# Optimization experiments

Hardware: AMD Instinct MI355X
Metric: run time of the kernel (lower is better)

The kernel has to match this reference:

```python
import jax, jax.numpy as jnp
import numpy as np

H = 16  # n_head

def _rotate_half(x):
    d = x.shape[-1] // 2
    return jnp.concatenate([-x[..., d:], x[..., :d]], axis=-1)

def setup_inputs() -> dict:
    key = jax.random.key(0)
    ks = jax.random.split(key, 12)
    b, t, f, h = 8, 1024, 1024, H
    d = f // h
    inp = {
        "query": jax.random.normal(ks[0], (b, t, f), jnp.float32),
        "key": jax.random.normal(ks[1], (b, t, f), jnp.float32),
        "value": jax.random.normal(ks[2], (b, t, f), jnp.float32),
    }
    # realistic rotary cos/sin, shape (t,1,1,d_k)
    inv_freq = 1.0 / (10000.0 ** (np.arange(0, d, 2, dtype=np.float32) / d))
    pos = np.arange(t, dtype=np.float32)[:, None] * inv_freq[None, :]  # (t, d/2)
    emb = np.concatenate([pos, pos], axis=-1)  # (t, d)
    inp["cos"] = jnp.asarray(np.cos(emb)).reshape(t, 1, 1, d)
    inp["sin"] = jnp.asarray(np.sin(emb)).reshape(t, 1, 1, d)
    inp["mask"] = jax.random.randint(ks[3], (b, t, t), 0, 2) > 0
    s = 1.0 / np.sqrt(f)
    inp["Wq"] = jax.random.normal(ks[4], (f, f), jnp.float32) * s
    inp["bq"] = jax.random.normal(ks[5], (f,), jnp.float32) * 0.02
    inp["Wk"] = jax.random.normal(ks[6], (f, f), jnp.float32) * s
    inp["bk"] = jax.random.normal(ks[7], (f,), jnp.float32) * 0.02
    inp["Wv"] = jax.random.normal(ks[8], (f, f), jnp.float32) * s
    inp["bv"] = jax.random.normal(ks[9], (f,), jnp.float32) * 0.02
    inp["Wo"] = jax.random.normal(ks[10], (f, f), jnp.float32) * s
    inp["bo"] = jax.random.normal(ks[11], (f,), jnp.float32) * 0.02
    return inp

def reference(query, key, value, cos, sin, mask, Wq, bq, Wk, bk, Wv, bv, Wo, bo):
    b, t, f = query.shape
    h = H
    d = f // h
    # RoPE applied pre-projection, per-head layout (b,t,h,d)
    c = cos.reshape(1, t, 1, d)  # broadcast over batch and heads
    s = sin.reshape(1, t, 1, d)
    qr = query.reshape(b, t, h, d)
    kr = key.reshape(b, t, h, d)
    qr = qr * c + _rotate_half(qr) * s
    kr = kr * c + _rotate_half(kr) * s
    q_in = qr.reshape(b, t, f)
    k_in = kr.reshape(b, t, f)
    # QKV projections (nn.Linear: x @ W.T + b), then split heads -> (b,h,t,d)
    q = (jnp.einsum('btf,gf->btg', q_in, Wq) + bq).reshape(b, t, h, d).transpose(0, 2, 1, 3)
    k = (jnp.einsum('btf,gf->btg', k_in, Wk) + bk).reshape(b, t, h, d).transpose(0, 2, 1, 3)
    v = (jnp.einsum('btf,gf->btg', value, Wv) + bv).reshape(b, t, h, d).transpose(0, 2, 1, 3)
    scores = jnp.einsum('bhqd,bhkd->bhqk', q, k) / jnp.sqrt(jnp.asarray(d, q.dtype))
    m = mask[:, None, :, :]  # (b,1,t,t)
    scores = jnp.where(m, jnp.asarray(-10000.0, scores.dtype), scores)
    attn = jax.nn.softmax(scores, axis=-1)
    attn = jnp.where(m, jnp.asarray(0.0, attn.dtype), attn)
    out = jnp.einsum('bhqk,bhkd->bhqd', attn, v)  # (b,h,t,d)
    out = out.transpose(0, 2, 1, 3).reshape(b, t, f)
    return jnp.einsum('btf,gf->btg', out, Wo) + bo
```

## Files before the change

kernel.cpp:

```cpp
#include <hip/hip_runtime.h>
#include <stdint.h>

typedef short short8 __attribute__((ext_vector_type(8)));
typedef float f32x4 __attribute__((ext_vector_type(4)));
typedef unsigned short ushort4v __attribute__((ext_vector_type(4)));
typedef unsigned int uint4v __attribute__((ext_vector_type(4)));
typedef unsigned long long u64;

#if __has_builtin(__builtin_amdgcn_exp2f)
#define EXP2(x) __builtin_amdgcn_exp2f(x)
#else
#define EXP2(x) exp2f(x)
#endif

__device__ __forceinline__ unsigned short f2bf(float f) {
  union { float f; unsigned u; } v; v.f = f;
  unsigned r = v.u + 0x7fffu + ((v.u >> 16) & 1u);
  return (unsigned short)(r >> 16);
}

__device__ __forceinline__ unsigned cvt_pk_bf16(float lo, float hi) {
  unsigned r;
  asm("v_cvt_pk_bf16_f32 %0, %1, %2" : "=v"(r) : "v"(lo), "v"(hi));
  return r;
}

__device__ __forceinline__ void gld_lds16(const void* g, void* l) {
  __builtin_amdgcn_global_load_lds((const __attribute__((address_space(1))) void*)g,
                                   (__attribute__((address_space(3))) void*)l, 16, 0, 0);
}

__global__ void mask_pack(const int* __restrict__ mask, u64* __restrict__ bits) {
  const int tid = blockIdx.x * 256 + threadIdx.x;
  const int w = tid >> 6, j = tid & 63;
  const int gh = w & 1, ktb = (w >> 1) & 7, bq = w >> 4;
  const int nt = (j >> 2) & 7, r = j & 3, g = gh * 2 + (j >> 5);
  const int k = nt * 16 + g * 4 + r;
  const int v = mask[(size_t)bq * 1024 + ktb * 128 + k];
  const u64 b = __ballot(v != 0);
  if (j == 0) bits[w] = b;
}

__global__ void rope_cast_kernel(const float* __restrict__ q, const float* __restrict__ k,
                                 const float* __restrict__ v,
                                 const float* __restrict__ cs, const float* __restrict__ sn,
                                 unsigned short* __restrict__ qo, unsigned short* __restrict__ ko,
                                 unsigned short* __restrict__ vo) {
  const int idx = blockIdx.x * 256 + threadIdx.x;
  const int p   = idx & 7;
  const int bth = idx >> 3;
  const int t   = (bth >> 4) & 1023;
  const size_t base = (size_t)bth * 64;
  const int dd0 = p * 4;

  const float4 x0 = *(const float4*)(q + base + dd0);
  const float4 x1 = *(const float4*)(q + base + dd0 + 32);
  const float4 y0 = *(const float4*)(k + base + dd0);
  const float4 y1 = *(const float4*)(k + base + dd0 + 32);
  const float4 c0 = *(const float4*)(cs + t * 64 + dd0);
  const float4 c1 = *(const float4*)(cs + t * 64 + dd0 + 32);
  const float4 s0 = *(const float4*)(sn + t * 64 + dd0);
  const float4 s1 = *(const float4*)(sn + t * 64 + dd0 + 32);

  ushort4v qlo, qhi, klo, khi;
  qlo[0]=f2bf(x0.x*c0.x - x1.x*s0.x); qlo[1]=f2bf(x0.y*c0.y - x1.y*s0.y);
  qlo[2]=f2bf(x0.z*c0.z - x1.z*s0.z); qlo[3]=f2bf(x0.w*c0.w - x1.w*s0.w);
  qhi[0]=f2bf(x1.x*c1.x + x0.x*s1.x); qhi[1]=f2bf(x1.y*c1.y + x0.y*s1.y);
  qhi[2]=f2bf(x1.z*c1.z + x0.z*s1.z); qhi[3]=f2bf(x1.w*c1.w + x0.w*s1.w);
  klo[0]=f2bf(y0.x*c0.x - y1.x*s0.x); klo[1]=f2bf(y0.y*c0.y - y1.y*s0.y);
  klo[2]=f2bf(y0.z*c0.z - y1.z*s0.z); klo[3]=f2bf(y0.w*c0.w - y1.w*s0.w);
  khi[0]=f2bf(y1.x*c1.x + y0.x*s1.x); khi[1]=f2bf(y1.y*c1.y + y0.y*s1.y);
  khi[2]=f2bf(y1.z*c1.z + y0.z*s1.z); khi[3]=f2bf(y1.w*c1.w + y0.w*s1.w);

  *(ushort4v*)(qo + base + dd0)      = qlo;
  *(ushort4v*)(qo + base + dd0 + 32) = qhi;
  *(ushort4v*)(ko + base + dd0)      = klo;
  *(ushort4v*)(ko + base + dd0 + 32) = khi;

  const size_t vb = (size_t)idx * 8;
  const float4 va = *(const float4*)(v + vb);
  const float4 vbv = *(const float4*)(v + vb + 4);
  ushort4v oa, ob;
  oa[0]=f2bf(va.x); oa[1]=f2bf(va.y); oa[2]=f2bf(va.z); oa[3]=f2bf(va.w);
  ob[0]=f2bf(vbv.x); ob[1]=f2bf(vbv.y); ob[2]=f2bf(vbv.z); ob[3]=f2bf(vbv.w);
  *(ushort4v*)(vo + vb)     = oa;
  *(ushort4v*)(vo + vb + 4) = ob;
}

__global__ void cast4_kernel(const float* __restrict__ s0, const float* __restrict__ s1,
                             const float* __restrict__ s2, const float* __restrict__ s3,
                             unsigned short* __restrict__ d0, unsigned short* __restrict__ d1,
                             unsigned short* __restrict__ d2, unsigned short* __restrict__ d3) {
  const int m = blockIdx.y;
  const float* src = (m == 0) ? s0 : (m == 1) ? s1 : (m == 2) ? s2 : s3;
  unsigned short* dst = (m == 0) ? d0 : (m == 1) ? d1 : (m == 2) ? d2 : d3;
  const int i = blockIdx.x * 256 + threadIdx.x;
  const float4 v = *(const float4*)(src + (size_t)i * 4);
  ushort4v o;
  o[0]=f2bf(v.x); o[1]=f2bf(v.y); o[2]=f2bf(v.z); o[3]=f2bf(v.w);
  *(ushort4v*)(dst + (size_t)i * 4) = o;
}

__global__ __launch_bounds__(256, 4) void gemm_qkv(
    const unsigned short* __restrict__ Aq, const unsigned short* __restrict__ Ak,
    const unsigned short* __restrict__ Av,
    const unsigned short* __restrict__ Bq, const unsigned short* __restrict__ Bk,
    const unsigned short* __restrict__ Bv,
    const float* __restrict__ bq, const float* __restrict__ bk, const float* __restrict__ bv,
    unsigned short* __restrict__ Cq, unsigned short* __restrict__ Ck,
    unsigned short* __restrict__ Cv) {
  constexpr int K = 1024;
  const int z = blockIdx.z;
  const unsigned short* A  = (z == 0) ? Aq : (z == 1) ? Ak : Av;
  const unsigned short* Bw = (z == 0) ? Bq : (z == 1) ? Bk : Bv;
  const float* bias        = (z == 0) ? bq : (z == 1) ? bk : bv;
  unsigned short* Co       = (z == 0) ? Cq : (z == 1) ? Ck : Cv;
  const float scale = (z == 0) ? 0.18033688f : 1.0f;

  const int tid = threadIdx.x;
  const int wave = tid >> 6, lane = tid & 63;
  const int m0 = blockIdx.x * 128, n0 = blockIdx.y * 128;
  __shared__ unsigned short Asm[128 * 64];
  __shared__ unsigned short Bsm[128 * 64];
  f32x4 acc[4][4] = {};
  const int wr = (wave >> 1) * 64, wc = (wave & 1) * 64;
  const int ld_row = lane >> 3;
  const int ld_col = ((lane & 7) ^ ld_row) * 8;
  const int fr = lane & 15, g = lane >> 4;
  const int fr7 = fr & 7;

  for (int k0 = 0; k0 < K; k0 += 64) {
#pragma unroll
    for (int j = 0; j < 4; ++j) {
      const int c = j * 4 + wave;
      gld_lds16(A  + (size_t)(m0 + 8 * c + ld_row) * K + k0 + ld_col, &Asm[c * 512]);
      gld_lds16(Bw + (size_t)(n0 + 8 * c + ld_row) * K + k0 + ld_col, &Bsm[c * 512]);
    }
    __syncthreads();
#pragma unroll
    for (int ks = 0; ks < 2; ++ks) {
      const int ch = ((ks * 4 + g) ^ fr7) * 8;
      short8 af[4], bf[4];
#pragma unroll
      for (int i = 0; i < 4; ++i)
        af[i] = *(const short8*)&Asm[(wr + i * 16 + fr) * 64 + ch];
#pragma unroll
      for (int i = 0; i < 4; ++i)
        bf[i] = *(const short8*)&Bsm[(wc + i * 16 + fr) * 64 + ch];
#pragma unroll
      for (int i = 0; i < 4; ++i)
#pragma unroll
        for (int j = 0; j < 4; ++j)
          acc[i][j] = __builtin_amdgcn_mfma_f32_16x16x32_bf16(af[i], bf[j], acc[i][j], 0, 0, 0);
    }
    __syncthreads();
  }

#pragma unroll
  for (int i = 0; i < 4; ++i) {
    const int row_base = m0 + wr + i * 16 + g * 4;
#pragma unroll
    for (int j = 0; j < 4; ++j) {
      const int col = n0 + wc + j * 16 + fr;
      const float bval = bias[col];
      const int h_i = col >> 6, dd = col & 63;
      if (z < 2) {
#pragma unroll
        for (int r = 0; r < 4; ++r) {
          const int row = row_base + r;
          const int b_i = row >> 10, t_i = row & 1023;
          Co[((size_t)(b_i * 16 + h_i) * 1024 + t_i) * 64 + dd] = f2bf((acc[i][j][r] + bval) * scale);
        }
      } else {
#pragma unroll
        for (int r = 0; r < 4; ++r) {
          const int row = row_base + r;
          const int b_i = row >> 10, t_i = row & 1023;
          const int kk = t_i & 127;
          const int kp = ((kk >> 4) & 3) * 32 + ((kk >> 2) & 3) * 8 + ((kk >> 6) & 1) * 4 + (kk & 3);
          Co[((size_t)(b_i * 16 + h_i) * 64 + dd) * 1024 + (t_i & ~127) + kp] =
              f2bf((acc[i][j][r] + bval));
        }
      }
    }
  }
}

__global__ __launch_bounds__(256, 2) void gemm_o(
    const unsigned short* __restrict__ A, const unsigned short* __restrict__ Bw,
    const float* __restrict__ bias, float* __restrict__ C) {
  constexpr int K = 1024, N = 1024;
  const int tid = threadIdx.x;
  const int wave = tid >> 6, lane = tid & 63;
  const int m0 = blockIdx.x * 128, n0 = blockIdx.y * 128;
  __shared__ unsigned short Asm[128 * 64];
  __shared__ unsigned short Bsm[128 * 64];
  f32x4 acc[4][4] = {};
  const int wr = (wave >> 1) * 64, wc = (wave & 1) * 64;
  const int ld_row = lane >> 3;
  const int ld_col = ((lane & 7) ^ ld_row) * 8;
  const int fr = lane & 15, g = lane >> 4;
  const int fr7 = fr & 7;

  for (int k0 = 0; k0 < K; k0 += 64) {
#pragma unroll
    for (int j = 0; j < 4; ++j) {
      const int c = j * 4 + wave;
      gld_lds16(A  + (size_t)(m0 + 8 * c + ld_row) * K + k0 + ld_col, &Asm[c * 512]);
      gld_lds16(Bw + (size_t)(n0 + 8 * c + ld_row) * K + k0 + ld_col, &Bsm[c * 512]);
    }
    __syncthreads();
#pragma unroll
    for (int ks = 0; ks < 2; ++ks) {
      const int ch = ((ks * 4 + g) ^ fr7) * 8;
      short8 af[4], bf[4];
#pragma unroll
      for (int i = 0; i < 4; ++i)
        af[i] = *(const short8*)&Asm[(wr + i * 16 + fr) * 64 + ch];
#pragma unroll
      for (int i = 0; i < 4; ++i)
        bf[i] = *(const short8*)&Bsm[(wc + i * 16 + fr) * 64 + ch];
#pragma unroll
      for (int i = 0; i < 4; ++i)
#pragma unroll
        for (int j = 0; j < 4; ++j)
          acc[i][j] = __builtin_amdgcn_mfma_f32_16x16x32_bf16(af[i], bf[j], acc[i][j], 0, 0, 0);
    }
    __syncthreads();
  }

#pragma unroll
  for (int i = 0; i < 4; ++i) {
    const int row_base = m0 + wr + i * 16 + g * 4;
#pragma unroll
    for (int j = 0; j < 4; ++j) {
      const int col = n0 + wc + j * 16 + fr;
      const float bval = bias[col];
#pragma unroll
      for (int r = 0; r < 4; ++r)
        C[(size_t)(row_base + r) * N + col] = acc[i][j][r] + bval;
    }
  }
}

__global__ __launch_bounds__(256, 2) void flash_attn(
    const unsigned short* __restrict__ Qp, const unsigned short* __restrict__ Kp,
    const unsigned short* __restrict__ Vp, const u64* __restrict__ mbits,
    unsigned short* __restrict__ O) {
  const int bh = blockIdx.x & 127, b_i = bh >> 4, h_i = bh & 15;
  const int q0 = (blockIdx.x >> 7) * 128;
  const int tid = threadIdx.x, wave = tid >> 6, lane = tid & 63;
  const unsigned short* Qb = Qp + (size_t)bh * 65536;
  const unsigned short* Kb = Kp + (size_t)bh * 65536;
  const unsigned short* Vb = Vp + (size_t)bh * 65536;
  const u64* mb = mbits + (size_t)b_i * 16384;

  __shared__ unsigned short smem[16384];
  unsigned short* Vsm = smem;
  unsigned short* Ksm = smem + 8192;

  const int fr = lane & 15, g = lane >> 4, fr7 = fr & 7;
  const int qw = q0 + wave * 32;

  short8 qf[2][2];
#pragma unroll
  for (int mt = 0; mt < 2; ++mt)
#pragma unroll
    for (int ks = 0; ks < 2; ++ks)
      qf[mt][ks] = *(const short8*)&Qb[(size_t)(qw + mt * 16 + fr) * 64 + ks * 32 + g * 8];

  f32x4 o_acc[2][4] = {};
  f32x4 o_l[2] = {};
  const short8 ones = {0x3F80, 0x3F80, 0x3F80, 0x3F80, 0x3F80, 0x3F80, 0x3F80, 0x3F80};

  const int kld_row = lane >> 3;
  const int kld_col = ((lane & 7) ^ kld_row) * 8;
  const int vld_row = lane >> 4;
  const int vld_r7w = 4 * (wave & 1) + vld_row;
  const int vld_col = ((lane & 15) ^ vld_r7w) * 8;

  for (int kt = 0; kt < 1024; kt += 128) {
#pragma unroll
    for (int j = 0; j < 4; ++j) {
      const int c = j * 4 + wave;
      gld_lds16(Kb + (size_t)(kt + 8 * c + kld_row) * 64 + kld_col, &Ksm[c * 512]);
      gld_lds16(Vb + (size_t)(4 * c + vld_row) * 1024 + kt + vld_col, &Vsm[c * 512]);
    }
    __syncthreads();

    f32x4 s_acc[2][8] = {};
#pragma unroll
    for (int ks = 0; ks < 2; ++ks) {
      const int ch = ((ks * 4 + g) ^ fr7) * 8;
      short8 kf[8];
#pragma unroll
      for (int nt = 0; nt < 8; ++nt)
        kf[nt] = *(const short8*)&Ksm[(nt * 16 + fr) * 64 + ch];
      __builtin_amdgcn_s_setprio(1);
#pragma unroll
      for (int mt = 0; mt < 2; ++mt)
#pragma unroll
        for (int nt = 0; nt < 8; ++nt)
          s_acc[mt][nt] = __builtin_amdgcn_mfma_f32_16x16x32_bf16(kf[nt], qf[mt][ks], s_acc[mt][nt], 0, 0, 0);
      __builtin_amdgcn_s_setprio(0);
    }

    short8 pf[2][4];
#pragma unroll
    for (int mt = 0; mt < 2; ++mt) {
      const u64 w = mb[(size_t)(qw + mt * 16 + fr) * 16 + (kt >> 7) * 2 + (g >> 1)];
      const unsigned bits = (unsigned)(w >> ((g & 1) * 32));
#pragma unroll
      for (int ks2 = 0; ks2 < 4; ++ks2) {
        float e[8];
#pragma unroll
        for (int r = 0; r < 4; ++r) {
          float a = EXP2(s_acc[mt][ks2][r]);
          a = (bits & (1u << (ks2 * 4 + r))) ? 0.0f : a;
          float b2 = EXP2(s_acc[mt][ks2 + 4][r]);
          b2 = (bits & (1u << (16 + ks2 * 4 + r))) ? 0.0f : b2;
          e[r] = a; e[4 + r] = b2;
        }
        uint4v pk;
        pk[0] = cvt_pk_bf16(e[0], e[1]);
        pk[1] = cvt_pk_bf16(e[2], e[3]);
        pk[2] = cvt_pk_bf16(e[4], e[5]);
        pk[3] = cvt_pk_bf16(e[6], e[7]);
        union { uint4v u; short8 s; } cv; cv.u = pk;
        pf[mt][ks2] = cv.s;
      }
    }

#pragma unroll
    for (int ks2 = 0; ks2 < 4; ++ks2) {
      const int cc = (ks2 * 4 + g) ^ fr7;
      short8 vf[4];
#pragma unroll
      for (int dt = 0; dt < 4; ++dt)
        vf[dt] = *(const short8*)&Vsm[(dt * 16 + fr) * 128 + cc * 8];
      __builtin_amdgcn_s_setprio(1);
#pragma unroll
      for (int mt = 0; mt < 2; ++mt) {
#pragma unroll
        for (int dt = 0; dt < 4; ++dt)
          o_acc[mt][dt] = __builtin_amdgcn_mfma_f32_16x16x32_bf16(pf[mt][ks2], vf[dt], o_acc[mt][dt], 0, 0, 0);
        o_l[mt] = __builtin_amdgcn_mfma_f32_16x16x32_bf16(pf[mt][ks2], ones, o_l[mt], 0, 0, 0);
      }
      __builtin_amdgcn_s_setprio(0);
    }
    __syncthreads();
  }

#pragma unroll
  for (int mt = 0; mt < 2; ++mt) {
#pragma unroll
    for (int r = 0; r < 4; ++r) {
      const float inv_l = 1.0f / o_l[mt][r];
      const int qrow = qw + mt * 16 + g * 4 + r;
#pragma unroll
      for (int dt = 0; dt < 4; ++dt) {
        const int dcol = dt * 16 + fr;
        O[((size_t)(b_i * 1024 + qrow)) * 1024 + h_i * 64 + dcol] = f2bf(o_acc[mt][dt][r] * inv_l);
      }
    }
  }
}

extern "C" void kernel_launch(void* const* d_in, const int* in_sizes, int n_in,
                              void* d_out, int out_size, void* d_ws, size_t ws_size,
                              hipStream_t stream) {
  const float* query = (const float*)d_in[0];
  const float* key   = (const float*)d_in[1];
  const float* value = (const float*)d_in[2];
  const float* cosb  = (const float*)d_in[3];
  const float* sinb  = (const float*)d_in[4];
  const int*   mask  = (const int*)d_in[5];
  const float* Wq = (const float*)d_in[6];
  const float* bq = (const float*)d_in[7];
  const float* Wk = (const float*)d_in[8];
  const float* bk = (const float*)d_in[9];
  const float* Wv = (const float*)d_in[10];
  const float* bv = (const float*)d_in[11];
  const float* Wo = (const float*)d_in[12];
  const float* bo = (const float*)d_in[13];
  (void)in_sizes; (void)n_in; (void)out_size; (void)ws_size;

  char* ws = (char*)d_ws;
  const size_t MB = 1024 * 1024;
  unsigned short* q_in = (unsigned short*)(ws);
  unsigned short* k_in = (unsigned short*)(ws + 16 * MB);
  unsigned short* v_bf = (unsigned short*)(ws + 32 * MB);
  unsigned short* Qp   = (unsigned short*)(ws + 48 * MB);
  unsigned short* Kp   = (unsigned short*)(ws + 64 * MB);
  unsigned short* Vp   = (unsigned short*)(ws + 80 * MB);
  unsigned short* Wqb  = (unsigned short*)(ws + 96 * MB);
  unsigned short* Wkb  = (unsigned short*)(ws + 98 * MB);
  unsigned short* Wvb  = (unsigned short*)(ws + 100 * MB);
  unsigned short* Wob  = (unsigned short*)(ws + 102 * MB);
  u64*            mbits= (u64*)(ws + 104 * MB);
  unsigned short* attn = q_in;

  mask_pack<<<32768, 256, 0, stream>>>(mask, mbits);
  rope_cast_kernel<<<4096, 256, 0, stream>>>(query, key, value, cosb, sinb, q_in, k_in, v_bf);
  cast4_kernel<<<dim3(1024, 4), 256, 0, stream>>>(Wq, Wk, Wv, Wo, Wqb, Wkb, Wvb, Wob);

  dim3 blk(256);
  gemm_qkv<<<dim3(64, 8, 3), blk, 0, stream>>>(q_in, k_in, v_bf, Wqb, Wkb, Wvb,
                                               bq, bk, bv, Qp, Kp, Vp);
  flash_attn<<<1024, blk, 0, stream>>>(Qp, Kp, Vp, mbits, attn);
  gemm_o<<<dim3(64, 8), blk, 0, stream>>>(attn, Wob, bo, (float*)d_out);
}
```

Measured before the change: 343.3 us.

## Fuse prep kernels, double-buffer K/V tiles in attention, raise gemm_o occupancy

Merges the mask packing, RoPE/cast and weight-cast kernels into a single launch to cut launch overhead and tail gaps. The flash attention kernel now double-buffers its K/V shared-memory tiles, prefetching the next tile with async global-to-LDS loads and using explicit waitcnt and barriers. It also loads the mask words earlier in each iteration. gemm_o's launch bounds rise to 4 waves per SIMD, which may force register spills, and doubling LDS in attention may lower its occupancy.

```diff
diff --git a/kernel.cpp b/kernel.cpp
--- a/kernel.cpp
+++ b/kernel.cpp
@@ -30,75 +30,77 @@
                                    (__attribute__((address_space(3))) void*)l, 16, 0, 0);
 }
 
-__global__ void mask_pack(const int* __restrict__ mask, u64* __restrict__ bits) {
-  const int tid = blockIdx.x * 256 + threadIdx.x;
-  const int w = tid >> 6, j = tid & 63;
-  const int gh = w & 1, ktb = (w >> 1) & 7, bq = w >> 4;
-  const int nt = (j >> 2) & 7, r = j & 3, g = gh * 2 + (j >> 5);
-  const int k = nt * 16 + g * 4 + r;
-  const int v = mask[(size_t)bq * 1024 + ktb * 128 + k];
-  const u64 b = __ballot(v != 0);
-  if (j == 0) bits[w] = b;
-}
-
-__global__ void rope_cast_kernel(const float* __restrict__ q, const float* __restrict__ k,
-                                 const float* __restrict__ v,
-                                 const float* __restrict__ cs, const float* __restrict__ sn,
-                                 unsigned short* __restrict__ qo, unsigned short* __restrict__ ko,
-                                 unsigned short* __restrict__ vo) {
-  const int idx = blockIdx.x * 256 + threadIdx.x;
-  const int p   = idx & 7;
-  const int bth = idx >> 3;
-  const int t   = (bth >> 4) & 1023;
-  const size_t base = (size_t)bth * 64;
-  const int dd0 = p * 4;
-
-  const float4 x0 = *(const float4*)(q + base + dd0);
-  const float4 x1 = *(const float4*)(q + base + dd0 + 32);
-  const float4 y0 = *(const float4*)(k + base + dd0);
-  const float4 y1 = *(const float4*)(k + base + dd0 + 32);
-  const float4 c0 = *(const float4*)(cs + t * 64 + dd0);
-  const float4 c1 = *(const float4*)(cs + t * 64 + dd0 + 32);
-  const float4 s0 = *(const float4*)(sn + t * 64 + dd0);
-  const float4 s1 = *(const float4*)(sn + t * 64 + dd0 + 32);
-
-  ushort4v qlo, qhi, klo, khi;
-  qlo[0]=f2bf(x0.x*c0.x - x1.x*s0.x); qlo[1]=f2bf(x0.y*c0.y - x1.y*s0.y);
-  qlo[2]=f2bf(x0.z*c0.z - x1.z*s0.z); qlo[3]=f2bf(x0.w*c0.w - x1.w*s0.w);
-  qhi[0]=f2bf(x1.x*c1.x + x0.x*s1.x); qhi[1]=f2bf(x1.y*c1.y + x0.y*s1.y);
-  qhi[2]=f2bf(x1.z*c1.z + x0.z*s1.z); qhi[3]=f2bf(x1.w*c1.w + x0.w*s1.w);
-  klo[0]=f2bf(y0.x*c0.x - y1.x*s0.x); klo[1]=f2bf(y0.y*c0.y - y1.y*s0.y);
-  klo[2]=f2bf(y0.z*c0.z - y1.z*s0.z); klo[3]=f2bf(y0.w*c0.w - y1.w*s0.w);
-  khi[0]=f2bf(y1.x*c1.x + y0.x*s1.x); khi[1]=f2bf(y1.y*c1.y + y0.y*s1.y);
-  khi[2]=f2bf(y1.z*c1.z + y0.z*s1.z); khi[3]=f2bf(y1.w*c1.w + y0.w*s1.w);
-
-  *(ushort4v*)(qo + base + dd0)      = qlo;
-  *(ushort4v*)(qo + base + dd0 + 32) = qhi;
-  *(ushort4v*)(ko + base + dd0)      = klo;
-  *(ushort4v*)(ko + base + dd0 + 32) = khi;
-
-  const size_t vb = (size_t)idx * 8;
-  const float4 va = *(const float4*)(v + vb);
-  const float4 vbv = *(const float4*)(v + vb + 4);
-  ushort4v oa, ob;
-  oa[0]=f2bf(va.x); oa[1]=f2bf(va.y); oa[2]=f2bf(va.z); oa[3]=f2bf(va.w);
-  ob[0]=f2bf(vbv.x); ob[1]=f2bf(vbv.y); ob[2]=f2bf(vbv.z); ob[3]=f2bf(vbv.w);
-  *(ushort4v*)(vo + vb)     = oa;
-  *(ushort4v*)(vo + vb + 4) = ob;
-}
-
-__global__ void cast4_kernel(const float* __restrict__ s0, const float* __restrict__ s1,
-                             const float* __restrict__ s2, const float* __restrict__ s3,
-                             unsigned short* __restrict__ d0, unsigned short* __restrict__ d1,
-                             unsigned short* __restrict__ d2, unsigned short* __restrict__ d3) {
-  const int m = blockIdx.y;
-  const float* src = (m == 0) ? s0 : (m == 1) ? s1 : (m == 2) ? s2 : s3;
-  unsigned short* dst = (m == 0) ? d0 : (m == 1) ? d1 : (m == 2) ? d2 : d3;
-  const int i = blockIdx.x * 256 + threadIdx.x;
-  const float4 v = *(const float4*)(src + (size_t)i * 4);
-  ushort4v o;
-  o[0]=f2bf(v.x); o[1]=f2bf(v.y); o[2]=f2bf(v.z); o[3]=f2bf(v.w);
-  *(ushort4v*)(dst + (size_t)i * 4) = o;
+__global__ void prep_kernel(const float* __restrict__ q, const float* __restrict__ k,
+                            const float* __restrict__ v,
+                            const float* __restrict__ cs, const float* __restrict__ sn,
+                            unsigned short* __restrict__ qo, unsigned short* __restrict__ ko,
+                            unsigned short* __restrict__ vo,
+                            const int* __restrict__ mask, u64* __restrict__ bits,
+                            const float* __restrict__ s0, const float* __restrict__ s1,
+                            const float* __restrict__ s2, const float* __restrict__ s3,
+                            unsigned short* __restrict__ d0, unsigned short* __restrict__ d1,
+                            unsigned short* __restrict__ d2, unsigned short* __restrict__ d3) {
+  const int bx = blockIdx.x;
+  if (bx < 4096) {
+    const int idx = bx * 256 + threadIdx.x;
+    const int p   = idx & 7;
+    const int bth = idx >> 3;
+    const int t   = (bth >> 4) & 1023;
+    const size_t base = (size_t)bth * 64;
+    const int dd0 = p * 4;
+
+    const float4 x0 = *(const float4*)(q + base + dd0);
+    const float4 x1 = *(const float4*)(q + base + dd0 + 32);
+    const float4 y0 = *(const float4*)(k + base + dd0);
+    const float4 y1 = *(const float4*)(k + base + dd0 + 32);
+    const float4 c0 = *(const float4*)(cs + t * 64 + dd0);
+    const float4 c1 = *(const float4*)(cs + t * 64 + dd0 + 32);
+    const float4 sl = *(const float4*)(sn + t * 64 + dd0);
+    const float4 sh = *(const float4*)(sn + t * 64 + dd0 + 32);
+
+    ushort4v qlo, qhi, klo, khi;
+    qlo[0]=f2bf(x0.x*c0.x - x1.x*sl.x); qlo[1]=f2bf(x0.y*c0.y - x1.y*sl.y);
+    qlo[2]=f2bf(x0.z*c0.z - x1.z*sl.z); qlo[3]=f2bf(x0.w*c0.w - x1.w*sl.w);
+    qhi[0]=f2bf(x1.x*c1.x + x0.x*sh.x); qhi[1]=f2bf(x1.y*c1.y + x0.y*sh.y);
+    qhi[2]=f2bf(x1.z*c1.z + x0.z*sh.z); qhi[3]=f2bf(x1.w*c1.w + x0.w*sh.w);
+    klo[0]=f2bf(y0.x*c0.x - y1.x*sl.x); klo[1]=f2bf(y0.y*c0.y - y1.y*sl.y);
+    klo[2]=f2bf(y0.z*c0.z - y1.z*sl.z); klo[3]=f2bf(y0.w*c0.w - y1.w*sl.w);
+    khi[0]=f2bf(y1.x*c1.x + y0.x*sh.x); khi[1]=f2bf(y1.y*c1.y + y0.y*sh.y);
+    khi[2]=f2bf(y1.z*c1.z + y0.z*sh.z); khi[3]=f2bf(y1.w*c1.w + y0.w*sh.w);
+
+    *(ushort4v*)(qo + base + dd0)      = qlo;
+    *(ushort4v*)(qo + base + dd0 + 32) = qhi;
+    *(ushort4v*)(ko + base + dd0)      = klo;
+    *(ushort4v*)(ko + base + dd0 + 32) = khi;
+
+    const size_t vb = (size_t)idx * 8;
+    const float4 va = *(const float4*)(v + vb);
+    const float4 vbv = *(const float4*)(v + vb + 4);
+    ushort4v oa, ob;
+    oa[0]=f2bf(va.x); oa[1]=f2bf(va.y); oa[2]=f2bf(va.z); oa[3]=f2bf(va.w);
+    ob[0]=f2bf(vbv.x); ob[1]=f2bf(vbv.y); ob[2]=f2bf(vbv.z); ob[3]=f2bf(vbv.w);
+    *(ushort4v*)(vo + vb)     = oa;
+    *(ushort4v*)(vo + vb + 4) = ob;
+  } else if (bx < 36864) {
+    const int tid = (bx - 4096) * 256 + threadIdx.x;
+    const int w = tid >> 6, j = tid & 63;
+    const int gh = w & 1, ktb = (w >> 1) & 7, bq = w >> 4;
+    const int nt = (j >> 2) & 7, r = j & 3, g = gh * 2 + (j >> 5);
+    const int kk = nt * 16 + g * 4 + r;
+    const int mv = mask[(size_t)bq * 1024 + ktb * 128 + kk];
+    const u64 b = __ballot(mv != 0);
+    if (j == 0) bits[w] = b;
+  } else {
+    const int idx2 = bx - 36864;
+    const int m = idx2 >> 10;
+    const float* src = (m == 0) ? s0 : (m == 1) ? s1 : (m == 2) ? s2 : s3;
+    unsigned short* dst = (m == 0) ? d0 : (m == 1) ? d1 : (m == 2) ? d2 : d3;
+    const int i = (idx2 & 1023) * 256 + threadIdx.x;
+    const float4 vv = *(const float4*)(src + (size_t)i * 4);
+    ushort4v o;
+    o[0]=f2bf(vv.x); o[1]=f2bf(vv.y); o[2]=f2bf(vv.z); o[3]=f2bf(vv.w);
+    *(ushort4v*)(dst + (size_t)i * 4) = o;
+  }
 }
 
 __global__ __launch_bounds__(256, 4) void gemm_qkv(
@@ -186,7 +188,7 @@
   }
 }
 
-__global__ __launch_bounds__(256, 2) void gemm_o(
+__global__ __launch_bounds__(256, 4) void gemm_o(
     const unsigned short* __restrict__ A, const unsigned short* __restrict__ Bw,
     const float* __restrict__ bias, float* __restrict__ C) {
   constexpr int K = 1024, N = 1024;
@@ -255,9 +257,7 @@
   const unsigned short* Vb = Vp + (size_t)bh * 65536;
   const u64* mb = mbits + (size_t)b_i * 16384;
 
-  __shared__ unsigned short smem[16384];
-  unsigned short* Vsm = smem;
-  unsigned short* Ksm = smem + 8192;
+  __shared__ unsigned short smem[32768];
 
   const int fr = lane & 15, g = lane >> 4, fr7 = fr & 7;
   const int qw = q0 + wave * 32;
@@ -279,14 +279,34 @@
   const int vld_r7w = 4 * (wave & 1) + vld_row;
   const int vld_col = ((lane & 15) ^ vld_r7w) * 8;
 
+#define STAGE(P, KT)                                                                     \
+  do {                                                                                   \
+    _Pragma("unroll")                                                                    \
+    for (int j = 0; j < 4; ++j) {                                                        \
+      const int c = j * 4 + wave;                                                        \
+      gld_lds16(Kb + (size_t)((KT) + 8 * c + kld_row) * 64 + kld_col,                    \
+                &smem[(P) * 16384 + 8192 + c * 512]);                                    \
+      gld_lds16(Vb + (size_t)(4 * c + vld_row) * 1024 + (KT) + vld_col,                  \
+                &smem[(P) * 16384 + c * 512]);                                           \
+    }                                                                                    \
+  } while (0)
+
+  STAGE(0, 0);
+  int p = 0;
   for (int kt = 0; kt < 1024; kt += 128) {
-#pragma unroll
-    for (int j = 0; j < 4; ++j) {
-      const int c = j * 4 + wave;
-      gld_lds16(Kb + (size_t)(kt + 8 * c + kld_row) * 64 + kld_col, &Ksm[c * 512]);
-      gld_lds16(Vb + (size_t)(4 * c + vld_row) * 1024 + kt + vld_col, &Vsm[c * 512]);
-    }
-    __syncthreads();
+    if (kt < 896) {
+      STAGE(p ^ 1, kt + 128);
+      asm volatile("s_waitcnt vmcnt(8)" ::: "memory");
+    } else {
+      asm volatile("s_waitcnt vmcnt(0)" ::: "memory");
+    }
+    __builtin_amdgcn_s_barrier();
+    asm volatile("" ::: "memory");
+    const unsigned short* Vsm = &smem[p * 16384];
+    const unsigned short* Ksm = &smem[p * 16384 + 8192];
+
+    const u64 w0 = mb[(size_t)(qw + fr) * 16 + (kt >> 7) * 2 + (g >> 1)];
+    const u64 w1 = mb[(size_t)(qw + 16 + fr) * 16 + (kt >> 7) * 2 + (g >> 1)];
 
     f32x4 s_acc[2][8] = {};
 #pragma unroll
@@ -308,7 +328,7 @@
     short8 pf[2][4];
 #pragma unroll
     for (int mt = 0; mt < 2; ++mt) {
-      const u64 w = mb[(size_t)(qw + mt * 16 + fr) * 16 + (kt >> 7) * 2 + (g >> 1)];
+      const u64 w = mt ? w1 : w0;
       const unsigned bits = (unsigned)(w >> ((g & 1) * 32));
 #pragma unroll
       for (int ks2 = 0; ks2 < 4; ++ks2) {
@@ -348,8 +368,11 @@
       }
       __builtin_amdgcn_s_setprio(0);
     }
-    __syncthreads();
-  }
+    asm volatile("" ::: "memory");
+    __builtin_amdgcn_s_barrier();
+    p ^= 1;
+  }
+#undef STAGE
 
 #pragma unroll
   for (int mt = 0; mt < 2; ++mt) {
@@ -400,9 +423,8 @@
   u64*            mbits= (u64*)(ws + 104 * MB);
   unsigned short* attn = q_in;
 
-  mask_pack<<<32768, 256, 0, stream>>>(mask, mbits);
-  rope_cast_kernel<<<4096, 256, 0, stream>>>(query, key, value, cosb, sinb, q_in, k_in, v_bf);
-  cast4_kernel<<<dim3(1024, 4), 256, 0, stream>>>(Wq, Wk, Wv, Wo, Wqb, Wkb, Wvb, Wob);
+  prep_kernel<<<40960, 256, 0, stream>>>(query, key, value, cosb, sinb, q_in, k_in, v_bf,
+                                         mask, mbits, Wq, Wk, Wv, Wo, Wqb, Wkb, Wvb, Wob);
 
   dim3 blk(256);
   gemm_qkv<<<dim3(64, 8, 3), blk, 0, stream>>>(q_in, k_in, v_bf, Wqb, Wkb, Wvb,
```

After: 345.9 us. Within noise of the previous version (+0.8%).
